# Kernel optimization log

Hardware: AMD Instinct MI355X
Metric: run time of the kernel (lower is better)

## Reference

```python
import jax, jax.numpy as jnp
import numpy as np
from jax import lax

N = 120000      # total real voxels
C = 128         # d_model
NH = 8          # heads
HD = C // NH    # head dim
T = 36          # window capacity
FILL = 24       # real tokens per window
NW = N // FILL  # 5000 windows
L = 4           # encoder layers (num_blocks=2, 2 layers each)
DFF = 256
B, H, Wd = 2, 320, 320
SCALE = HD ** -0.5


def setup_inputs() -> dict:
    key = jax.random.key(0)
    ks = jax.random.split(key, 16)
    voxel_feats = jax.random.normal(ks[0], (N, C), jnp.float32)
    # shift-0 window assignment: contiguous; shift-1: random permutation of voxels
    base = jnp.arange(N, dtype=jnp.int32)
    ind0 = (base // FILL) * T + (base % FILL)
    perm = jax.random.permutation(ks[1], N).astype(jnp.int32)
    ind1 = (perm // FILL) * T + (perm % FILL)
    mask = jnp.tile(jnp.arange(T) >= FILL, (NW, 1))  # True = padded key slot
    pos0 = 0.02 * jax.random.normal(ks[2], (NW, T, C), jnp.float32)
    pos1 = 0.02 * jax.random.normal(ks[3], (NW, T, C), jnp.float32)
    bcol = (jnp.arange(N) >= N // 2).astype(jnp.int32)
    yy = jax.random.randint(ks[4], (N,), 0, H, jnp.int32)
    xx = jax.random.randint(ks[5], (N,), 0, Wd, jnp.int32)
    voxel_coors = jnp.stack([bcol, jnp.zeros(N, jnp.int32), yy, xx], axis=1)
    s = 0.02
    return dict(
        voxel_feats=voxel_feats,
        pos0=pos0, pos1=pos1,
        in_proj_w=s * jax.random.normal(ks[6], (L, 3 * C, C), jnp.float32),
        in_proj_b=jnp.zeros((L, 3 * C), jnp.float32),
        out_proj_w=s * jax.random.normal(ks[7], (L, C, C), jnp.float32),
        out_proj_b=jnp.zeros((L, C), jnp.float32),
        lin1_w=s * jax.random.normal(ks[8], (L, DFF, C), jnp.float32),
        lin1_b=jnp.zeros((L, DFF), jnp.float32),
        lin2_w=s * jax.random.normal(ks[9], (L, C, DFF), jnp.float32),
        lin2_b=jnp.zeros((L, C), jnp.float32),
        ln1_w=jnp.ones((L, C), jnp.float32), ln1_b=jnp.zeros((L, C), jnp.float32),
        ln2_w=jnp.ones((L, C), jnp.float32), ln2_b=jnp.zeros((L, C), jnp.float32),
        conv_w=0.05 * jax.random.normal(ks[10], (2, C, C, 3, 3), jnp.float32),
        voxel_coors=voxel_coors, ind0=ind0, ind1=ind1, mask0=mask, mask1=mask,
    )


def _ln(x, w, b):
    m = jnp.mean(x, -1, keepdims=True)
    v = jnp.mean((x - m) ** 2, -1, keepdims=True)
    return (x - m) * lax.rsqrt(v + 1e-5) * w + b


def _encoder_layer(x, ind, pos, mask, ipw, ipb, opw, opb, l1w, l1b, l2w, l2b,
                   n1w, n1b, n2w, n2b):
    # flat2window_v2: scatter flat tokens into padded window buffer
    feat3d = jnp.zeros((NW * T, C), x.dtype).at[ind].set(x).reshape(NW, T, C)
    qk_in = feat3d + pos  # pos added to q and k only
    wq, wk, wv = ipw[:C], ipw[C:2 * C], ipw[2 * C:]
    bq, bk, bv = ipb[:C], ipb[C:2 * C], ipb[2 * C:]
    q = (qk_in @ wq.T + bq).reshape(NW, T, NH, HD)
    k = (qk_in @ wk.T + bk).reshape(NW, T, NH, HD)
    v = (feat3d @ wv.T + bv).reshape(NW, T, NH, HD)
    scores = jnp.einsum('wqhd,wkhd->whqk', q, k) * SCALE
    scores = jnp.where(mask[:, None, None, :], -1e9, scores)  # key padding mask
    attn = jax.nn.softmax(scores, axis=-1)
    o = jnp.einsum('whqk,wkhd->wqhd', attn, v).reshape(NW, T, C)
    o = o @ opw.T + opb
    a = o.reshape(NW * T, C)[ind]  # window2flat_v2: gather valid slots
    x = _ln(x + a, n1w, n1b)       # post_norm residual 1
    f = jax.nn.gelu(x @ l1w.T + l1b, approximate=False) @ l2w.T + l2b
    return _ln(x + f, n2w, n2b)    # post_norm residual 2


def reference(voxel_feats, pos0, pos1, in_proj_w, in_proj_b, out_proj_w,
              out_proj_b, lin1_w, lin1_b, lin2_w, lin2_b, ln1_w, ln1_b,
              ln2_w, ln2_b, conv_w, voxel_coors, ind0, ind1, mask0, mask1):
    x = voxel_feats
    for l in range(L):
        ind, pos, mask = (ind0, pos0, mask0) if l % 2 == 0 else (ind1, pos1, mask1)
        x = _encoder_layer(x, ind, pos, mask, in_proj_w[l], in_proj_b[l],
                           out_proj_w[l], out_proj_b[l], lin1_w[l], lin1_b[l],
                           lin2_w[l], lin2_b[l], ln1_w[l], ln1_b[l],
                           ln2_w[l], ln2_b[l])
    # recover_bev: scatter tokens into dense [B, C, H, W] canvas
    flat = voxel_coors[:, 2] * Wd + voxel_coors[:, 3]
    canvas = jnp.zeros((B, H * Wd, C), x.dtype).at[voxel_coors[:, 0], flat].set(x)
    out = canvas.reshape(B, H, Wd, C).transpose(0, 3, 1, 2)
    for i in range(2):  # attached 3x3 conv (bias=False) + ReLU
        out = jax.nn.relu(lax.conv_general_dilated(
            out, conv_w[i], (1, 1), [(1, 1), (1, 1)],
            dimension_numbers=('NCHW', 'OIHW', 'NCHW')))
    return out
```

## Files before the change

### kernel.cpp

```cpp
#include <hip/hip_runtime.h>
#include <math.h>

#define NVOX 120000
#define CDIM 128
#define NWIN 5000
#define HWPIX 102400

typedef __attribute__((ext_vector_type(8))) short short8;
typedef __attribute__((ext_vector_type(4))) float f32x4;

__device__ __forceinline__ unsigned short f2bf(float f) {
  unsigned u = __float_as_uint(f);
  return (unsigned short)((u + 0x7FFFu + ((u >> 16) & 1u)) >> 16);
}
__device__ __forceinline__ unsigned pack2(float a, float b) {
  return (unsigned)f2bf(a) | ((unsigned)f2bf(b) << 16);
}
__device__ __forceinline__ void unpack2(unsigned u, float& a, float& b) {
  a = __uint_as_float(u << 16);
  b = __uint_as_float(u & 0xFFFF0000u);
}

__device__ __forceinline__ void mma128(const short* __restrict__ As,
                                       const short* __restrict__ Ws,
                                       int aoff, int boff, f32x4 acc[2][4]) {
#pragma unroll
  for (int kc = 0; kc < 4; ++kc) {
    short8 a0 = *(const short8*)(As + aoff + kc * 32);
    short8 a1 = *(const short8*)(As + aoff + 136 * 16 + kc * 32);
#pragma unroll
    for (int nt = 0; nt < 4; ++nt) {
      short8 b = *(const short8*)(Ws + boff + nt * 136 * 16 + kc * 32);
      acc[0][nt] = __builtin_amdgcn_mfma_f32_16x16x32_bf16(a0, b, acc[0][nt], 0, 0, 0);
      acc[1][nt] = __builtin_amdgcn_mfma_f32_16x16x32_bf16(a1, b, acc[1][nt], 0, 0, 0);
    }
  }
}

__global__ __launch_bounds__(256) void cvt_kernel(const float* __restrict__ src,
                                                  unsigned short* __restrict__ dst, int n4) {
  int i = blockIdx.x * 256 + threadIdx.x;
  if (i >= n4) return;
  float4 v = ((const float4*)src)[i];
  uint2 o; o.x = pack2(v.x, v.y); o.y = pack2(v.z, v.w);
  ((uint2*)dst)[i] = o;
}

__global__ __launch_bounds__(256) void cvtT_kernel(const float* __restrict__ w,
                                                   unsigned short* __restrict__ wT) {
  int idx = blockIdx.x * 256 + threadIdx.x;
  if (idx >= 2 * 9 * 128 * 128) return;
  int ci = idx & 127;
  int co = (idx >> 7) & 127;
  int tap = (idx >> 14) % 9;
  int conv = idx / (9 * 16384);
  wT[idx] = f2bf(w[((size_t)(conv * 128 + co) * 128 + ci) * 9 + tap]);
}

__global__ __launch_bounds__(256) void qkv_kernel(
    const unsigned short* __restrict__ x, const float* __restrict__ pos,
    const int* __restrict__ ind, const unsigned short* __restrict__ ipwB,
    const float* __restrict__ ipb, unsigned short* __restrict__ qb,
    unsigned short* __restrict__ kb, unsigned short* __restrict__ vb) {
  __shared__ __align__(16) char ldsraw[52224];
  short* As = (short*)ldsraw;
  short* Ws = (short*)(ldsraw + 17408);
  const int t = threadIdx.x;
  const int lane = t & 63, wv = t >> 6;
  const int l15 = lane & 15, quad = lane >> 4;
  const int rbase = 32 * (wv >> 1), cbase = 64 * (wv & 1);
  const int mbase = blockIdx.x * 64;
  const int sec = blockIdx.y;
  f32x4 acc[2][4];
#pragma unroll
  for (int m = 0; m < 2; ++m)
#pragma unroll
    for (int n = 0; n < 4; ++n) acc[m][n] = (f32x4){0.f, 0.f, 0.f, 0.f};

  for (int fi = t; fi < 1024; fi += 256) {
    int row = fi >> 4, c8 = fi & 15;
    int vox = mbase + row;
    uint4 xv = ((const uint4*)x)[(size_t)vox * 16 + c8];
    if (sec < 2) {
      int s = ind[vox];
      const float4* pp = (const float4*)(pos + (size_t)s * 128 + c8 * 8);
      float4 p0 = pp[0], p1 = pp[1];
      float f0, f1, f2, f3, f4, f5, f6, f7;
      unpack2(xv.x, f0, f1); unpack2(xv.y, f2, f3);
      unpack2(xv.z, f4, f5); unpack2(xv.w, f6, f7);
      xv.x = pack2(f0 + p0.x, f1 + p0.y); xv.y = pack2(f2 + p0.z, f3 + p0.w);
      xv.z = pack2(f4 + p1.x, f5 + p1.y); xv.w = pack2(f6 + p1.z, f7 + p1.w);
    }
    *(uint4*)&As[row * 136 + c8 * 8] = xv;
  }
  for (int fi = t; fi < 2048; fi += 256) {
    int row = fi >> 4, c8 = fi & 15;
    ((uint4*)&Ws[row * 136])[c8] =
        ((const uint4*)(ipwB + (size_t)(sec * 128 + row) * 128))[c8];
  }
  __syncthreads();
  mma128(As, Ws, (rbase + l15) * 136 + quad * 8, (cbase + l15) * 136 + quad * 8, acc);
  __syncthreads();

  short* Ybf = (short*)ldsraw;
#pragma unroll
  for (int nt = 0; nt < 4; ++nt) {
    int col = cbase + nt * 16 + l15;
    float bias = ipb[sec * 128 + col];
#pragma unroll
    for (int mt = 0; mt < 2; ++mt)
#pragma unroll
      for (int r = 0; r < 4; ++r)
        Ybf[(rbase + mt * 16 + quad * 4 + r) * 136 + col] =
            (short)f2bf(acc[mt][nt][r] + bias);
  }
  __syncthreads();
  unsigned short* dst = (sec == 0) ? qb : ((sec == 1) ? kb : vb);
  for (int fi = t; fi < 1024; fi += 256) {
    int row = fi >> 4, c8 = fi & 15;
    int s = ind[mbase + row];
    int slot = (s / 36) * 24 + (s % 36);
    ((uint4*)dst)[(size_t)slot * 16 + c8] = ((const uint4*)&Ybf[row * 136])[c8];
  }
}

__global__ __launch_bounds__(256) void attn_kernel(
    unsigned short* __restrict__ qb, const unsigned short* __restrict__ kb,
    const unsigned short* __restrict__ vb) {
  __shared__ float lds[14112];
  float* Qs = lds;
  float* Ks = lds + 3168;
  float* Vs = lds + 6336;
  float* S = lds + 9504;
  const int t = threadIdx.x;
  const size_t base = (size_t)blockIdx.x * 3072;
  for (int fi = t; fi < 1152; fi += 256) {
    int arr = fi / 384, rem = fi % 384;
    int row = rem >> 4, c8 = rem & 15;
    const unsigned short* src = arr == 0 ? qb : (arr == 1 ? kb : vb);
    uint4 raw = ((const uint4*)(src + base))[row * 16 + c8];
    float* dl = lds + arr * 3168 + row * 132 + c8 * 8;
    unpack2(raw.x, dl[0], dl[1]); unpack2(raw.y, dl[2], dl[3]);
    unpack2(raw.z, dl[4], dl[5]); unpack2(raw.w, dl[6], dl[7]);
  }
  __syncthreads();
  for (int idx = t; idx < 4608; idx += 256) {
    int hh = idx / 576, rem = idx % 576;
    int qq = rem / 24, kk = rem % 24;
    const float* qp = &Qs[qq * 132 + hh * 16];
    const float* kp = &Ks[kk * 132 + hh * 16];
    float s = 0.f;
#pragma unroll
    for (int d = 0; d < 16; ++d) s = fmaf(qp[d], kp[d], s);
    S[idx] = s * 0.25f;
  }
  __syncthreads();
  if (t < 192) {
    float* rowp = &S[t * 24];
    float m = rowp[0];
#pragma unroll
    for (int k2 = 1; k2 < 24; ++k2) m = fmaxf(m, rowp[k2]);
    float sum = 0.f;
#pragma unroll
    for (int k2 = 0; k2 < 24; ++k2) { float e = __expf(rowp[k2] - m); rowp[k2] = e; sum += e; }
    float inv = 1.f / sum;
#pragma unroll
    for (int k2 = 0; k2 < 24; ++k2) rowp[k2] *= inv;
  }
  __syncthreads();
  for (int idx = t; idx < 3072; idx += 256) {
    int hh = idx / 384, rem = idx % 384;
    int qq = rem >> 4, dd = rem & 15;
    const float* pp = &S[hh * 576 + qq * 24];
    const float* vp = &Vs[hh * 16 + dd];
    float o = 0.f;
#pragma unroll
    for (int k2 = 0; k2 < 24; ++k2) o = fmaf(pp[k2], vp[k2 * 132], o);
    qb[base + qq * 128 + hh * 16 + dd] = f2bf(o);
  }
}

__global__ __launch_bounds__(256) void outln_kernel(
    const unsigned short* __restrict__ o, const int* __restrict__ ind,
    const unsigned short* __restrict__ opwB, const float* __restrict__ opb,
    const unsigned short* __restrict__ xres, const float* __restrict__ lnw,
    const float* __restrict__ lnb, unsigned short* __restrict__ hout) {
  __shared__ __align__(16) char ldsraw[52224];
  short* As = (short*)ldsraw;
  short* Ws = (short*)(ldsraw + 17408);
  const int t = threadIdx.x;
  const int lane = t & 63, wv = t >> 6;
  const int l15 = lane & 15, quad = lane >> 4;
  const int rbase = 32 * (wv >> 1), cbase = 64 * (wv & 1);
  const int mbase = blockIdx.x * 64;
  f32x4 acc[2][4];
#pragma unroll
  for (int m = 0; m < 2; ++m)
#pragma unroll
    for (int n = 0; n < 4; ++n) acc[m][n] = (f32x4){0.f, 0.f, 0.f, 0.f};

  for (int fi = t; fi < 1024; fi += 256) {
    int row = fi >> 4, c8 = fi & 15;
    int s = ind[mbase + row];
    int slot = (s / 36) * 24 + (s % 36);
    *(uint4*)&As[row * 136 + c8 * 8] = ((const uint4*)o)[(size_t)slot * 16 + c8];
  }
  for (int fi = t; fi < 2048; fi += 256) {
    int row = fi >> 4, c8 = fi & 15;
    ((uint4*)&Ws[row * 136])[c8] = ((const uint4*)(opwB + (size_t)row * 128))[c8];
  }
  __syncthreads();
  mma128(As, Ws, (rbase + l15) * 136 + quad * 8, (cbase + l15) * 136 + quad * 8, acc);
  __syncthreads();

  float* Yf = (float*)ldsraw;
  float* p1 = (float*)(ldsraw + 33792);
  float* p2 = (float*)(ldsraw + 34816);
  float* Ms = (float*)(ldsraw + 35840);
  float* Rs = (float*)(ldsraw + 36096);
#pragma unroll
  for (int nt = 0; nt < 4; ++nt) {
    int col = cbase + nt * 16 + l15;
    float bias = opb[col];
#pragma unroll
    for (int mt = 0; mt < 2; ++mt)
#pragma unroll
      for (int r = 0; r < 4; ++r)
        Yf[(rbase + mt * 16 + quad * 4 + r) * 132 + col] = acc[mt][nt][r] + bias;
  }
  __syncthreads();
  for (int fi = t; fi < 1024; fi += 256) {
    int row = fi >> 4, c8 = fi & 15;
    uint4 xv = ((const uint4*)xres)[(size_t)(mbase + row) * 16 + c8];
    float* yp = &Yf[row * 132 + c8 * 8];
    float a, b;
    unpack2(xv.x, a, b); yp[0] += a; yp[1] += b;
    unpack2(xv.y, a, b); yp[2] += a; yp[3] += b;
    unpack2(xv.z, a, b); yp[4] += a; yp[5] += b;
    unpack2(xv.w, a, b); yp[6] += a; yp[7] += b;
  }
  __syncthreads();
  {
    int r = t & 63, g = t >> 6;
    float s = 0.f, s2 = 0.f;
    for (int c = g * 32; c < g * 32 + 32; ++c) { float v = Yf[r * 132 + c]; s += v; s2 += v * v; }
    p1[g * 64 + r] = s; p2[g * 64 + r] = s2;
  }
  __syncthreads();
  if (t < 64) {
    float s = p1[t] + p1[64 + t] + p1[128 + t] + p1[192 + t];
    float s2 = p2[t] + p2[64 + t] + p2[128 + t] + p2[192 + t];
    float m = s * (1.f / 128.f);
    float var = s2 * (1.f / 128.f) - m * m;
    Ms[t] = m; Rs[t] = rsqrtf(var + 1e-5f);
  }
  __syncthreads();
  for (int fi = t; fi < 1024; fi += 256) {
    int row = fi >> 4, c8 = fi & 15;
    float m = Ms[row], rr = Rs[row];
    const float* yp = &Yf[row * 132 + c8 * 8];
    uint4 ov;
    float v0, v1;
#define LNPAIR(J, FLD) \
    v0 = (yp[2*J] - m) * rr * lnw[c8*8+2*J] + lnb[c8*8+2*J]; \
    v1 = (yp[2*J+1] - m) * rr * lnw[c8*8+2*J+1] + lnb[c8*8+2*J+1]; \
    ov.FLD = pack2(v0, v1);
    LNPAIR(0, x) LNPAIR(1, y) LNPAIR(2, z) LNPAIR(3, w)
#undef LNPAIR
    ((uint4*)hout)[(size_t)(mbase + row) * 16 + c8] = ov;
  }
}

__global__ __launch_bounds__(256) void ffn1_kernel(
    const unsigned short* __restrict__ h, const unsigned short* __restrict__ w1B,
    const float* __restrict__ b1, unsigned short* __restrict__ ff) {
  __shared__ __align__(16) char ldsraw[52224];
  short* As = (short*)ldsraw;
  short* Ws = (short*)(ldsraw + 17408);
  const int t = threadIdx.x;
  const int lane = t & 63, wv = t >> 6;
  const int l15 = lane & 15, quad = lane >> 4;
  const int rbase = 32 * (wv >> 1), cbase = 64 * (wv & 1);
  const int mbase = blockIdx.x * 64;
  const int by = blockIdx.y;
  f32x4 acc[2][4];
#pragma unroll
  for (int m = 0; m < 2; ++m)
#pragma unroll
    for (int n = 0; n < 4; ++n) acc[m][n] = (f32x4){0.f, 0.f, 0.f, 0.f};

  for (int fi = t; fi < 1024; fi += 256) {
    int row = fi >> 4, c8 = fi & 15;
    *(uint4*)&As[row * 136 + c8 * 8] = ((const uint4*)h)[(size_t)(mbase + row) * 16 + c8];
  }
  for (int fi = t; fi < 2048; fi += 256) {
    int row = fi >> 4, c8 = fi & 15;
    ((uint4*)&Ws[row * 136])[c8] =
        ((const uint4*)(w1B + (size_t)(by * 128 + row) * 128))[c8];
  }
  __syncthreads();
  mma128(As, Ws, (rbase + l15) * 136 + quad * 8, (cbase + l15) * 136 + quad * 8, acc);
  __syncthreads();

  short* Ybf = (short*)ldsraw;
#pragma unroll
  for (int nt = 0; nt < 4; ++nt) {
    int col = cbase + nt * 16 + l15;
    float bias = b1[by * 128 + col];
#pragma unroll
    for (int mt = 0; mt < 2; ++mt)
#pragma unroll
      for (int r = 0; r < 4; ++r) {
        float v = acc[mt][nt][r] + bias;
        float g = 0.5f * v * (1.f + erff(v * 0.70710678f));
        Ybf[(rbase + mt * 16 + quad * 4 + r) * 136 + col] = (short)f2bf(g);
      }
  }
  __syncthreads();
  for (int fi = t; fi < 1024; fi += 256) {
    int row = fi >> 4, c8 = fi & 15;
    ((uint4*)ff)[(size_t)(mbase + row) * 32 + by * 16 + c8] =
        ((const uint4*)&Ybf[row * 136])[c8];
  }
}

__global__ __launch_bounds__(256) void ffn2_kernel(
    const unsigned short* __restrict__ ff, const unsigned short* __restrict__ w2B,
    const float* __restrict__ b2, const unsigned short* __restrict__ hres,
    const float* __restrict__ lnw, const float* __restrict__ lnb,
    unsigned short* __restrict__ xout) {
  __shared__ __align__(16) char ldsraw[52224];
  short* As = (short*)ldsraw;
  short* Ws = (short*)(ldsraw + 17408);
  const int t = threadIdx.x;
  const int lane = t & 63, wv = t >> 6;
  const int l15 = lane & 15, quad = lane >> 4;
  const int rbase = 32 * (wv >> 1), cbase = 64 * (wv & 1);
  const int mbase = blockIdx.x * 64;
  f32x4 acc[2][4];
#pragma unroll
  for (int m = 0; m < 2; ++m)
#pragma unroll
    for (int n = 0; n < 4; ++n) acc[m][n] = (f32x4){0.f, 0.f, 0.f, 0.f};

  for (int k2 = 0; k2 < 2; ++k2) {
    if (k2) __syncthreads();
    for (int fi = t; fi < 1024; fi += 256) {
      int row = fi >> 4, c8 = fi & 15;
      *(uint4*)&As[row * 136 + c8 * 8] =
          ((const uint4*)ff)[(size_t)(mbase + row) * 32 + k2 * 16 + c8];
    }
    for (int fi = t; fi < 2048; fi += 256) {
      int row = fi >> 4, c8 = fi & 15;
      ((uint4*)&Ws[row * 136])[c8] =
          ((const uint4*)(w2B + (size_t)row * 256 + k2 * 128))[c8];
    }
    __syncthreads();
    mma128(As, Ws, (rbase + l15) * 136 + quad * 8, (cbase + l15) * 136 + quad * 8, acc);
  }
  __syncthreads();

  float* Yf = (float*)ldsraw;
  float* p1 = (float*)(ldsraw + 33792);
  float* p2 = (float*)(ldsraw + 34816);
  float* Ms = (float*)(ldsraw + 35840);
  float* Rs = (float*)(ldsraw + 36096);
#pragma unroll
  for (int nt = 0; nt < 4; ++nt) {
    int col = cbase + nt * 16 + l15;
    float bias = b2[col];
#pragma unroll
    for (int mt = 0; mt < 2; ++mt)
#pragma unroll
      for (int r = 0; r < 4; ++r)
        Yf[(rbase + mt * 16 + quad * 4 + r) * 132 + col] = acc[mt][nt][r] + bias;
  }
  __syncthreads();
  for (int fi = t; fi < 1024; fi += 256) {
    int row = fi >> 4, c8 = fi & 15;
    uint4 xv = ((const uint4*)hres)[(size_t)(mbase + row) * 16 + c8];
    float* yp = &Yf[row * 132 + c8 * 8];
    float a, b;
    unpack2(xv.x, a, b); yp[0] += a; yp[1] += b;
    unpack2(xv.y, a, b); yp[2] += a; yp[3] += b;
    unpack2(xv.z, a, b); yp[4] += a; yp[5] += b;
    unpack2(xv.w, a, b); yp[6] += a; yp[7] += b;
  }
  __syncthreads();
  {
    int r = t & 63, g = t >> 6;
    float s = 0.f, s2 = 0.f;
    for (int c = g * 32; c < g * 32 + 32; ++c) { float v = Yf[r * 132 + c]; s += v; s2 += v * v; }
    p1[g * 64 + r] = s; p2[g * 64 + r] = s2;
  }
  __syncthreads();
  if (t < 64) {
    float s = p1[t] + p1[64 + t] + p1[128 + t] + p1[192 + t];
    float s2 = p2[t] + p2[64 + t] + p2[128 + t] + p2[192 + t];
    float m = s * (1.f / 128.f);
    float var = s2 * (1.f / 128.f) - m * m;
    Ms[t] = m; Rs[t] = rsqrtf(var + 1e-5f);
  }
  __syncthreads();
  for (int fi = t; fi < 1024; fi += 256) {
    int row = fi >> 4, c8 = fi & 15;
    float m = Ms[row], rr = Rs[row];
    const float* yp = &Yf[row * 132 + c8 * 8];
    uint4 ov;
    float v0, v1;
#define LNPAIR(J, FLD) \
    v0 = (yp[2*J] - m) * rr * lnw[c8*8+2*J] + lnb[c8*8+2*J]; \
    v1 = (yp[2*J+1] - m) * rr * lnw[c8*8+2*J+1] + lnb[c8*8+2*J+1]; \
    ov.FLD = pack2(v0, v1);
    LNPAIR(0, x) LNPAIR(1, y) LNPAIR(2, z) LNPAIR(3, w)
#undef LNPAIR
    ((uint4*)xout)[(size_t)(mbase + row) * 16 + c8] = ov;
  }
}

__global__ void idx_init_kernel(int* __restrict__ idxmap) {
  int i = blockIdx.x * 256 + threadIdx.x;
  if (i < 2 * HWPIX) idxmap[i] = -1;
}

__global__ void scatter_kernel(const int* __restrict__ coors, int* __restrict__ idxmap) {
  int i = blockIdx.x * 256 + threadIdx.x;
  if (i >= NVOX) return;
  int b = coors[i * 4 + 0], y = coors[i * 4 + 2], xx = coors[i * 4 + 3];
  atomicMax(&idxmap[b * HWPIX + y * 320 + xx], i);
}

__global__ void canvas_kernel(const unsigned short* __restrict__ x,
                              const int* __restrict__ idxmap,
                              unsigned short* __restrict__ canvas) {
  int idx = blockIdx.x * 256 + threadIdx.x;
  if (idx >= 2 * HWPIX * 16) return;
  int cell = idx >> 4, c8 = idx & 15;
  int vox = idxmap[cell];
  uint4 v = {0u, 0u, 0u, 0u};
  if (vox >= 0) v = ((const uint4*)x)[(size_t)vox * 16 + c8];
  ((uint4*)canvas)[idx] = v;
}

template <int NCHW_OUT>
__global__ __launch_bounds__(256) void conv_kernel(
    const unsigned short* __restrict__ in, const unsigned short* __restrict__ wTb,
    void* __restrict__ outp) {
  __shared__ __align__(16) char ldsraw[52768];
  short* patch = (short*)ldsraw;
  short* Wt = (short*)(ldsraw + 17952);
  const int t = threadIdx.x;
  const int lane = t & 63, wv = t >> 6;
  const int l15 = lane & 15, quad = lane >> 4;
  const int rbase = 32 * (wv >> 1), cbase = 64 * (wv & 1);
  const int x0 = blockIdx.x * 64;
  const int y = blockIdx.y;
  const int b = blockIdx.z;
  const unsigned short* inb = in + (size_t)b * HWPIX * 128;
  f32x4 acc[2][4];
#pragma unroll
  for (int m = 0; m < 2; ++m)
#pragma unroll
    for (int n = 0; n < 4; ++n) acc[m][n] = (f32x4){0.f, 0.f, 0.f, 0.f};

  for (int dy = 0; dy < 3; ++dy) {
    __syncthreads();
    int gy = y + dy - 1;
    for (int fi = t; fi < 1056; fi += 256) {
      int col = fi >> 4, c8 = fi & 15;
      int gx = x0 + col - 1;
      uint4 v = {0u, 0u, 0u, 0u};
      if (gy >= 0 && gy < 320 && gx >= 0 && gx < 320)
        v = ((const uint4*)inb)[(size_t)(gy * 320 + gx) * 16 + c8];
      *(uint4*)&patch[col * 136 + c8 * 8] = v;
    }
    for (int dx = 0; dx < 3; ++dx) {
      __syncthreads();
      int tap = dy * 3 + dx;
      for (int fi = t; fi < 2048; fi += 256) {
        int row = fi >> 4, c8 = fi & 15;
        ((uint4*)&Wt[row * 136])[c8] =
            ((const uint4*)(wTb + (size_t)(tap * 128 + row) * 128))[c8];
      }
      __syncthreads();
      mma128(patch, Wt, (rbase + l15 + dx) * 136 + quad * 8,
             (cbase + l15) * 136 + quad * 8, acc);
    }
  }
  __syncthreads();
  if (NCHW_OUT) {
    float* Yf = (float*)ldsraw;
#pragma unroll
    for (int nt = 0; nt < 4; ++nt) {
      int col = cbase + nt * 16 + l15;
#pragma unroll
      for (int mt = 0; mt < 2; ++mt)
#pragma unroll
        for (int r = 0; r < 4; ++r)
          Yf[col * 68 + rbase + mt * 16 + quad * 4 + r] = fmaxf(acc[mt][nt][r], 0.f);
    }
    __syncthreads();
    float* out = (float*)outp;
    for (int fi = t; fi < 2048; fi += 256) {
      int co = fi >> 4, q4 = fi & 15;
      float4 v = *(float4*)&Yf[co * 68 + q4 * 4];
      *(float4*)&out[(size_t)(b * 128 + co) * HWPIX + y * 320 + x0 + q4 * 4] = v;
    }
  } else {
    short* Ybf = (short*)ldsraw;
#pragma unroll
    for (int nt = 0; nt < 4; ++nt) {
      int col = cbase + nt * 16 + l15;
#pragma unroll
      for (int mt = 0; mt < 2; ++mt)
#pragma unroll
        for (int r = 0; r < 4; ++r)
          Ybf[(rbase + mt * 16 + quad * 4 + r) * 136 + col] =
              (short)f2bf(fmaxf(acc[mt][nt][r], 0.f));
    }
    __syncthreads();
    unsigned short* out = (unsigned short*)outp;
    for (int fi = t; fi < 1024; fi += 256) {
      int row = fi >> 4, c8 = fi & 15;
      ((uint4*)out)[((size_t)b * HWPIX + y * 320 + x0 + row) * 16 + c8] =
          ((const uint4*)&Ybf[row * 136])[c8];
    }
  }
}

extern "C" void kernel_launch(void* const* d_in, const int* in_sizes, int n_in,
                              void* d_out, int out_size, void* d_ws, size_t ws_size,
                              hipStream_t stream) {
  const float* voxel_feats = (const float*)d_in[0];
  const float* pos0 = (const float*)d_in[1];
  const float* pos1 = (const float*)d_in[2];
  const float* ipw = (const float*)d_in[3];
  const float* ipb = (const float*)d_in[4];
  const float* opw = (const float*)d_in[5];
  const float* opb = (const float*)d_in[6];
  const float* l1w = (const float*)d_in[7];
  const float* l1b = (const float*)d_in[8];
  const float* l2w = (const float*)d_in[9];
  const float* l2b = (const float*)d_in[10];
  const float* n1w = (const float*)d_in[11];
  const float* n1b = (const float*)d_in[12];
  const float* n2w = (const float*)d_in[13];
  const float* n2b = (const float*)d_in[14];
  const float* convw = (const float*)d_in[15];
  const int* coors = (const int*)d_in[16];
  const int* ind0 = (const int*)d_in[17];
  const int* ind1 = (const int*)d_in[18];

  unsigned short* ws = (unsigned short*)d_ws;
  const size_t NC = (size_t)NVOX * CDIM;
  unsigned short* bx = ws;
  unsigned short* bq = ws + NC;
  unsigned short* bk = ws + 2 * NC;
  unsigned short* bv = ws + 3 * NC;
  unsigned short* bh = ws + 4 * NC;
  unsigned short* bff = ws + 5 * NC;
  unsigned short* wB = ws + 7 * NC;
  unsigned short* ipwB = wB;
  unsigned short* opwB = wB + 196608;
  unsigned short* l1wB = wB + 262144;
  unsigned short* l2wB = wB + 393216;
  unsigned short* convB = wB + 524288;
  int* idxmap = (int*)(wB + 819200);
  unsigned short* canvas = bq;
  unsigned short* c1out = bv;

  cvt_kernel<<<15000, 256, 0, stream>>>(voxel_feats, bx, 3840000);
  cvt_kernel<<<192, 256, 0, stream>>>(ipw, ipwB, 49152);
  cvt_kernel<<<64, 256, 0, stream>>>(opw, opwB, 16384);
  cvt_kernel<<<128, 256, 0, stream>>>(l1w, l1wB, 32768);
  cvt_kernel<<<128, 256, 0, stream>>>(l2w, l2wB, 32768);
  cvtT_kernel<<<1152, 256, 0, stream>>>(convw, convB);

  for (int l = 0; l < 4; ++l) {
    const int* ind = (l & 1) ? ind1 : ind0;
    const float* pos = (l & 1) ? pos1 : pos0;
    qkv_kernel<<<dim3(1875, 3), 256, 0, stream>>>(
        bx, pos, ind, ipwB + (size_t)l * 49152, ipb + l * 384, bq, bk, bv);
    attn_kernel<<<NWIN, 256, 0, stream>>>(bq, bk, bv);
    outln_kernel<<<1875, 256, 0, stream>>>(
        bq, ind, opwB + (size_t)l * 16384, opb + l * 128, bx,
        n1w + l * 128, n1b + l * 128, bh);
    ffn1_kernel<<<dim3(1875, 2), 256, 0, stream>>>(
        bh, l1wB + (size_t)l * 32768, l1b + l * 256, bff);
    ffn2_kernel<<<1875, 256, 0, stream>>>(
        bff, l2wB + (size_t)l * 32768, l2b + l * 128, bh,
        n2w + l * 128, n2b + l * 128, bx);
  }

  idx_init_kernel<<<800, 256, 0, stream>>>(idxmap);
  scatter_kernel<<<(NVOX + 255) / 256, 256, 0, stream>>>(coors, idxmap);
  canvas_kernel<<<12800, 256, 0, stream>>>(bx, idxmap, canvas);

  conv_kernel<0><<<dim3(5, 320, 2), 256, 0, stream>>>(canvas, convB, (void*)c1out);
  conv_kernel<1><<<dim3(5, 320, 2), 256, 0, stream>>>(c1out, convB + 9 * 16384, d_out);
}
```

Before: 1.610 ms.

## Loop QKV/FFN1 sections in-block, fuse attention per row, prefetch conv tiles

Several changes land together. The QKV and FFN1 kernels now loop over their output sections inside one block, so the activation tile is loaded once and the grid shrinks. Attention keeps scores in registers, with one thread per query/head doing QK, softmax and PV, which removes the LDS score buffer and two barriers. The conv kernel prefetches the next tap's weights and the next input row into registers while MFMA runs on the current ones. The cost is fewer blocks (less parallelism), only 192 active threads in attention, and higher register pressure in conv.

```diff
diff --git a/kernel.cpp b/kernel.cpp
--- a/kernel.cpp
+++ b/kernel.cpp
@@ -21,18 +21,23 @@
   b = __uint_as_float(u & 0xFFFF0000u);
 }
 
-__device__ __forceinline__ void mma128(const short* __restrict__ As,
-                                       const short* __restrict__ Ws,
-                                       int aoff, int boff, f32x4 acc[2][4]) {
+template <int MT>
+__device__ __forceinline__ void mma_k128(const short* __restrict__ As,
+                                         const short* __restrict__ Ws,
+                                         int aoff, int astride, int boff,
+                                         f32x4 acc[MT][4]) {
 #pragma unroll
   for (int kc = 0; kc < 4; ++kc) {
-    short8 a0 = *(const short8*)(As + aoff + kc * 32);
-    short8 a1 = *(const short8*)(As + aoff + 136 * 16 + kc * 32);
+    short8 a[MT];
+#pragma unroll
+    for (int mt = 0; mt < MT; ++mt)
+      a[mt] = *(const short8*)(As + aoff + mt * astride + kc * 32);
 #pragma unroll
     for (int nt = 0; nt < 4; ++nt) {
       short8 b = *(const short8*)(Ws + boff + nt * 136 * 16 + kc * 32);
-      acc[0][nt] = __builtin_amdgcn_mfma_f32_16x16x32_bf16(a0, b, acc[0][nt], 0, 0, 0);
-      acc[1][nt] = __builtin_amdgcn_mfma_f32_16x16x32_bf16(a1, b, acc[1][nt], 0, 0, 0);
+#pragma unroll
+      for (int mt = 0; mt < MT; ++mt)
+        acc[mt][nt] = __builtin_amdgcn_mfma_f32_16x16x32_bf16(a[mt], b, acc[mt][nt], 0, 0, 0);
     }
   }
 }
@@ -62,80 +67,90 @@
     const int* __restrict__ ind, const unsigned short* __restrict__ ipwB,
     const float* __restrict__ ipb, unsigned short* __restrict__ qb,
     unsigned short* __restrict__ kb, unsigned short* __restrict__ vb) {
-  __shared__ __align__(16) char ldsraw[52224];
+  __shared__ __align__(16) char ldsraw[52480];
   short* As = (short*)ldsraw;
   short* Ws = (short*)(ldsraw + 17408);
+  int* slots = (int*)(ldsraw + 52224);
   const int t = threadIdx.x;
   const int lane = t & 63, wv = t >> 6;
   const int l15 = lane & 15, quad = lane >> 4;
   const int rbase = 32 * (wv >> 1), cbase = 64 * (wv & 1);
   const int mbase = blockIdx.x * 64;
-  const int sec = blockIdx.y;
-  f32x4 acc[2][4];
-#pragma unroll
-  for (int m = 0; m < 2; ++m)
-#pragma unroll
-    for (int n = 0; n < 4; ++n) acc[m][n] = (f32x4){0.f, 0.f, 0.f, 0.f};
-
+
+  if (t < 64) {
+    int s = ind[mbase + t];
+    slots[t] = (s / 36) * 24 + (s % 36);
+  }
   for (int fi = t; fi < 1024; fi += 256) {
     int row = fi >> 4, c8 = fi & 15;
     int vox = mbase + row;
     uint4 xv = ((const uint4*)x)[(size_t)vox * 16 + c8];
-    if (sec < 2) {
-      int s = ind[vox];
-      const float4* pp = (const float4*)(pos + (size_t)s * 128 + c8 * 8);
-      float4 p0 = pp[0], p1 = pp[1];
-      float f0, f1, f2, f3, f4, f5, f6, f7;
-      unpack2(xv.x, f0, f1); unpack2(xv.y, f2, f3);
-      unpack2(xv.z, f4, f5); unpack2(xv.w, f6, f7);
-      xv.x = pack2(f0 + p0.x, f1 + p0.y); xv.y = pack2(f2 + p0.z, f3 + p0.w);
-      xv.z = pack2(f4 + p1.x, f5 + p1.y); xv.w = pack2(f6 + p1.z, f7 + p1.w);
-    }
+    int s = ind[vox];
+    const float4* pp = (const float4*)(pos + (size_t)s * 128 + c8 * 8);
+    float4 p0 = pp[0], p1 = pp[1];
+    float f0, f1, f2, f3, f4, f5, f6, f7;
+    unpack2(xv.x, f0, f1); unpack2(xv.y, f2, f3);
+    unpack2(xv.z, f4, f5); unpack2(xv.w, f6, f7);
+    xv.x = pack2(f0 + p0.x, f1 + p0.y); xv.y = pack2(f2 + p0.z, f3 + p0.w);
+    xv.z = pack2(f4 + p1.x, f5 + p1.y); xv.w = pack2(f6 + p1.z, f7 + p1.w);
     *(uint4*)&As[row * 136 + c8 * 8] = xv;
   }
-  for (int fi = t; fi < 2048; fi += 256) {
-    int row = fi >> 4, c8 = fi & 15;
-    ((uint4*)&Ws[row * 136])[c8] =
-        ((const uint4*)(ipwB + (size_t)(sec * 128 + row) * 128))[c8];
-  }
-  __syncthreads();
-  mma128(As, Ws, (rbase + l15) * 136 + quad * 8, (cbase + l15) * 136 + quad * 8, acc);
-  __syncthreads();
-
-  short* Ybf = (short*)ldsraw;
-#pragma unroll
-  for (int nt = 0; nt < 4; ++nt) {
-    int col = cbase + nt * 16 + l15;
-    float bias = ipb[sec * 128 + col];
-#pragma unroll
-    for (int mt = 0; mt < 2; ++mt)
-#pragma unroll
-      for (int r = 0; r < 4; ++r)
-        Ybf[(rbase + mt * 16 + quad * 4 + r) * 136 + col] =
-            (short)f2bf(acc[mt][nt][r] + bias);
-  }
-  __syncthreads();
-  unsigned short* dst = (sec == 0) ? qb : ((sec == 1) ? kb : vb);
-  for (int fi = t; fi < 1024; fi += 256) {
-    int row = fi >> 4, c8 = fi & 15;
-    int s = ind[mbase + row];
-    int slot = (s / 36) * 24 + (s % 36);
-    ((uint4*)dst)[(size_t)slot * 16 + c8] = ((const uint4*)&Ybf[row * 136])[c8];
+
+  for (int sec = 0; sec < 3; ++sec) {
+    if (sec == 2) {
+      for (int fi = t; fi < 1024; fi += 256) {
+        int row = fi >> 4, c8 = fi & 15;
+        *(uint4*)&As[row * 136 + c8 * 8] =
+            ((const uint4*)x)[(size_t)(mbase + row) * 16 + c8];
+      }
+    }
+    for (int fi = t; fi < 2048; fi += 256) {
+      int row = fi >> 4, c8 = fi & 15;
+      ((uint4*)&Ws[row * 136])[c8] =
+          ((const uint4*)(ipwB + (size_t)(sec * 128 + row) * 128))[c8];
+    }
+    __syncthreads();
+    f32x4 acc[2][4];
+#pragma unroll
+    for (int m = 0; m < 2; ++m)
+#pragma unroll
+      for (int n = 0; n < 4; ++n) acc[m][n] = (f32x4){0.f, 0.f, 0.f, 0.f};
+    mma_k128<2>(As, Ws, (rbase + l15) * 136 + quad * 8, 16 * 136,
+                (cbase + l15) * 136 + quad * 8, acc);
+    __syncthreads();
+    short* Ybf = Ws;
+#pragma unroll
+    for (int nt = 0; nt < 4; ++nt) {
+      int col = cbase + nt * 16 + l15;
+      float bias = ipb[sec * 128 + col];
+#pragma unroll
+      for (int mt = 0; mt < 2; ++mt)
+#pragma unroll
+        for (int r = 0; r < 4; ++r)
+          Ybf[(rbase + mt * 16 + quad * 4 + r) * 136 + col] =
+              (short)f2bf(acc[mt][nt][r] + bias);
+    }
+    __syncthreads();
+    unsigned short* dst = (sec == 0) ? qb : ((sec == 1) ? kb : vb);
+    for (int fi = t; fi < 1024; fi += 256) {
+      int row = fi >> 4, c8 = fi & 15;
+      ((uint4*)dst)[(size_t)slots[row] * 16 + c8] = ((const uint4*)&Ybf[row * 136])[c8];
+    }
+    __syncthreads();
   }
 }
 
 __global__ __launch_bounds__(256) void attn_kernel(
     unsigned short* __restrict__ qb, const unsigned short* __restrict__ kb,
     const unsigned short* __restrict__ vb) {
-  __shared__ float lds[14112];
+  __shared__ float lds[9504];
   float* Qs = lds;
   float* Ks = lds + 3168;
   float* Vs = lds + 6336;
-  float* S = lds + 9504;
   const int t = threadIdx.x;
   const size_t base = (size_t)blockIdx.x * 3072;
   for (int fi = t; fi < 1152; fi += 256) {
-    int arr = fi / 384, rem = fi % 384;
+    int arr = fi / 384, rem = fi - arr * 384;
     int row = rem >> 4, c8 = rem & 15;
     const unsigned short* src = arr == 0 ? qb : (arr == 1 ? kb : vb);
     uint4 raw = ((const uint4*)(src + base))[row * 16 + c8];
@@ -144,39 +159,55 @@
     unpack2(raw.z, dl[4], dl[5]); unpack2(raw.w, dl[6], dl[7]);
   }
   __syncthreads();
-  for (int idx = t; idx < 4608; idx += 256) {
-    int hh = idx / 576, rem = idx % 576;
-    int qq = rem / 24, kk = rem % 24;
-    const float* qp = &Qs[qq * 132 + hh * 16];
-    const float* kp = &Ks[kk * 132 + hh * 16];
-    float s = 0.f;
-#pragma unroll
-    for (int d = 0; d < 16; ++d) s = fmaf(qp[d], kp[d], s);
-    S[idx] = s * 0.25f;
-  }
-  __syncthreads();
   if (t < 192) {
-    float* rowp = &S[t * 24];
-    float m = rowp[0];
-#pragma unroll
-    for (int k2 = 1; k2 < 24; ++k2) m = fmaxf(m, rowp[k2]);
+    int h = t / 24, q = t - h * 24;
+    const float4* qp = (const float4*)&Qs[q * 132 + h * 16];
+    float4 q0 = qp[0], q1 = qp[1], q2 = qp[2], q3 = qp[3];
+    float sc[24];
+#pragma unroll
+    for (int k = 0; k < 24; ++k) {
+      const float4* kp = (const float4*)&Ks[k * 132 + h * 16];
+      float4 k0 = kp[0], k1 = kp[1], k2 = kp[2], k3 = kp[3];
+      float s = 0.f;
+      s = fmaf(q0.x, k0.x, s); s = fmaf(q0.y, k0.y, s);
+      s = fmaf(q0.z, k0.z, s); s = fmaf(q0.w, k0.w, s);
+      s = fmaf(q1.x, k1.x, s); s = fmaf(q1.y, k1.y, s);
+      s = fmaf(q1.z, k1.z, s); s = fmaf(q1.w, k1.w, s);
+      s = fmaf(q2.x, k2.x, s); s = fmaf(q2.y, k2.y, s);
+      s = fmaf(q2.z, k2.z, s); s = fmaf(q2.w, k2.w, s);
+      s = fmaf(q3.x, k3.x, s); s = fmaf(q3.y, k3.y, s);
+      s = fmaf(q3.z, k3.z, s); s = fmaf(q3.w, k3.w, s);
+      sc[k] = s * 0.25f;
+    }
+    float m = sc[0];
+#pragma unroll
+    for (int k = 1; k < 24; ++k) m = fmaxf(m, sc[k]);
     float sum = 0.f;
 #pragma unroll
-    for (int k2 = 0; k2 < 24; ++k2) { float e = __expf(rowp[k2] - m); rowp[k2] = e; sum += e; }
+    for (int k = 0; k < 24; ++k) { sc[k] = __expf(sc[k] - m); sum += sc[k]; }
     float inv = 1.f / sum;
-#pragma unroll
-    for (int k2 = 0; k2 < 24; ++k2) rowp[k2] *= inv;
-  }
-  __syncthreads();
-  for (int idx = t; idx < 3072; idx += 256) {
-    int hh = idx / 384, rem = idx % 384;
-    int qq = rem >> 4, dd = rem & 15;
-    const float* pp = &S[hh * 576 + qq * 24];
-    const float* vp = &Vs[hh * 16 + dd];
-    float o = 0.f;
-#pragma unroll
-    for (int k2 = 0; k2 < 24; ++k2) o = fmaf(pp[k2], vp[k2 * 132], o);
-    qb[base + qq * 128 + hh * 16 + dd] = f2bf(o);
+    float4 o0 = {0,0,0,0}, o1 = o0, o2 = o0, o3 = o0;
+#pragma unroll
+    for (int k = 0; k < 24; ++k) {
+      float p = sc[k] * inv;
+      const float4* vp = (const float4*)&Vs[k * 132 + h * 16];
+      float4 v0 = vp[0], v1 = vp[1], v2 = vp[2], v3 = vp[3];
+      o0.x = fmaf(p, v0.x, o0.x); o0.y = fmaf(p, v0.y, o0.y);
+      o0.z = fmaf(p, v0.z, o0.z); o0.w = fmaf(p, v0.w, o0.w);
+      o1.x = fmaf(p, v1.x, o1.x); o1.y = fmaf(p, v1.y, o1.y);
+      o1.z = fmaf(p, v1.z, o1.z); o1.w = fmaf(p, v1.w, o1.w);
+      o2.x = fmaf(p, v2.x, o2.x); o2.y = fmaf(p, v2.y, o2.y);
+      o2.z = fmaf(p, v2.z, o2.z); o2.w = fmaf(p, v2.w, o2.w);
+      o3.x = fmaf(p, v3.x, o3.x); o3.y = fmaf(p, v3.y, o3.y);
+      o3.z = fmaf(p, v3.z, o3.z); o3.w = fmaf(p, v3.w, o3.w);
+    }
+    uint4 lo, hi;
+    lo.x = pack2(o0.x, o0.y); lo.y = pack2(o0.z, o0.w);
+    lo.z = pack2(o1.x, o1.y); lo.w = pack2(o1.z, o1.w);
+    hi.x = pack2(o2.x, o2.y); hi.y = pack2(o2.z, o2.w);
+    hi.z = pack2(o3.x, o3.y); hi.w = pack2(o3.z, o3.w);
+    ((uint4*)(qb + base))[q * 16 + h * 2] = lo;
+    ((uint4*)(qb + base))[q * 16 + h * 2 + 1] = hi;
   }
 }
 
@@ -210,7 +241,8 @@
     ((uint4*)&Ws[row * 136])[c8] = ((const uint4*)(opwB + (size_t)row * 128))[c8];
   }
   __syncthreads();
-  mma128(As, Ws, (rbase + l15) * 136 + quad * 8, (cbase + l15) * 136 + quad * 8, acc);
+  mma_k128<2>(As, Ws, (rbase + l15) * 136 + quad * 8, 16 * 136,
+              (cbase + l15) * 136 + quad * 8, acc);
   __syncthreads();
 
   float* Yf = (float*)ldsraw;
@@ -282,45 +314,47 @@
   const int l15 = lane & 15, quad = lane >> 4;
   const int rbase = 32 * (wv >> 1), cbase = 64 * (wv & 1);
   const int mbase = blockIdx.x * 64;
-  const int by = blockIdx.y;
-  f32x4 acc[2][4];
-#pragma unroll
-  for (int m = 0; m < 2; ++m)
-#pragma unroll
-    for (int n = 0; n < 4; ++n) acc[m][n] = (f32x4){0.f, 0.f, 0.f, 0.f};
 
   for (int fi = t; fi < 1024; fi += 256) {
     int row = fi >> 4, c8 = fi & 15;
     *(uint4*)&As[row * 136 + c8 * 8] = ((const uint4*)h)[(size_t)(mbase + row) * 16 + c8];
   }
-  for (int fi = t; fi < 2048; fi += 256) {
-    int row = fi >> 4, c8 = fi & 15;
-    ((uint4*)&Ws[row * 136])[c8] =
-        ((const uint4*)(w1B + (size_t)(by * 128 + row) * 128))[c8];
-  }
-  __syncthreads();
-  mma128(As, Ws, (rbase + l15) * 136 + quad * 8, (cbase + l15) * 136 + quad * 8, acc);
-  __syncthreads();
-
-  short* Ybf = (short*)ldsraw;
-#pragma unroll
-  for (int nt = 0; nt < 4; ++nt) {
-    int col = cbase + nt * 16 + l15;
-    float bias = b1[by * 128 + col];
-#pragma unroll
-    for (int mt = 0; mt < 2; ++mt)
-#pragma unroll
-      for (int r = 0; r < 4; ++r) {
-        float v = acc[mt][nt][r] + bias;
-        float g = 0.5f * v * (1.f + erff(v * 0.70710678f));
-        Ybf[(rbase + mt * 16 + quad * 4 + r) * 136 + col] = (short)f2bf(g);
-      }
-  }
-  __syncthreads();
-  for (int fi = t; fi < 1024; fi += 256) {
-    int row = fi >> 4, c8 = fi & 15;
-    ((uint4*)ff)[(size_t)(mbase + row) * 32 + by * 16 + c8] =
-        ((const uint4*)&Ybf[row * 136])[c8];
+  for (int by = 0; by < 2; ++by) {
+    for (int fi = t; fi < 2048; fi += 256) {
+      int row = fi >> 4, c8 = fi & 15;
+      ((uint4*)&Ws[row * 136])[c8] =
+          ((const uint4*)(w1B + (size_t)(by * 128 + row) * 128))[c8];
+    }
+    __syncthreads();
+    f32x4 acc[2][4];
+#pragma unroll
+    for (int m = 0; m < 2; ++m)
+#pragma unroll
+      for (int n = 0; n < 4; ++n) acc[m][n] = (f32x4){0.f, 0.f, 0.f, 0.f};
+    mma_k128<2>(As, Ws, (rbase + l15) * 136 + quad * 8, 16 * 136,
+                (cbase + l15) * 136 + quad * 8, acc);
+    __syncthreads();
+    short* Ybf = Ws;
+#pragma unroll
+    for (int nt = 0; nt < 4; ++nt) {
+      int col = cbase + nt * 16 + l15;
+      float bias = b1[by * 128 + col];
+#pragma unroll
+      for (int mt = 0; mt < 2; ++mt)
+#pragma unroll
+        for (int r = 0; r < 4; ++r) {
+          float v = acc[mt][nt][r] + bias;
+          float g = 0.5f * v * (1.f + erff(v * 0.70710678f));
+          Ybf[(rbase + mt * 16 + quad * 4 + r) * 136 + col] = (short)f2bf(g);
+        }
+    }
+    __syncthreads();
+    for (int fi = t; fi < 1024; fi += 256) {
+      int row = fi >> 4, c8 = fi & 15;
+      ((uint4*)ff)[(size_t)(mbase + row) * 32 + by * 16 + c8] =
+          ((const uint4*)&Ybf[row * 136])[c8];
+    }
+    __syncthreads();
   }
 }
 
@@ -356,7 +390,8 @@
           ((const uint4*)(w2B + (size_t)row * 256 + k2 * 128))[c8];
     }
     __syncthreads();
-    mma128(As, Ws, (rbase + l15) * 136 + quad * 8, (cbase + l15) * 136 + quad * 8, acc);
+    mma_k128<2>(As, Ws, (rbase + l15) * 136 + quad * 8, 16 * 136,
+                (cbase + l15) * 136 + quad * 8, acc);
   }
   __syncthreads();
 
@@ -448,7 +483,7 @@
     void* __restrict__ outp) {
   __shared__ __align__(16) char ldsraw[52768];
   short* patch = (short*)ldsraw;
-  short* Wt = (short*)(ldsraw + 17952);
+  short* Ws = (short*)(ldsraw + 17952);
   const int t = threadIdx.x;
   const int lane = t & 63, wv = t >> 6;
   const int l15 = lane & 15, quad = lane >> 4;
@@ -463,31 +498,80 @@
 #pragma unroll
     for (int n = 0; n < 4; ++n) acc[m][n] = (f32x4){0.f, 0.f, 0.f, 0.f};
 
+  uint4 wreg[8], preg[5];
+#pragma unroll
+  for (int u = 0; u < 8; ++u) {
+    int fi = t + 256 * u;
+    wreg[u] = ((const uint4*)(wTb + (size_t)(fi >> 4) * 128))[fi & 15];
+  }
+  {
+    int gy = y - 1;
+#pragma unroll
+    for (int u = 0; u < 5; ++u) {
+      int fi = t + 256 * u;
+      preg[u] = (uint4){0u, 0u, 0u, 0u};
+      if (fi < 1056) {
+        int gx = x0 + (fi >> 4) - 1;
+        if (gy >= 0 && gy < 320 && gx >= 0 && gx < 320)
+          preg[u] = ((const uint4*)inb)[(size_t)(gy * 320 + gx) * 16 + (fi & 15)];
+      }
+    }
+  }
+#pragma unroll
+  for (int u = 0; u < 8; ++u) {
+    int fi = t + 256 * u;
+    *(uint4*)&Ws[(fi >> 4) * 136 + (fi & 15) * 8] = wreg[u];
+  }
+#pragma unroll
+  for (int u = 0; u < 5; ++u) {
+    int fi = t + 256 * u;
+    if (fi < 1056) *(uint4*)&patch[(fi >> 4) * 136 + (fi & 15) * 8] = preg[u];
+  }
+  __syncthreads();
+
   for (int dy = 0; dy < 3; ++dy) {
-    __syncthreads();
-    int gy = y + dy - 1;
-    for (int fi = t; fi < 1056; fi += 256) {
-      int col = fi >> 4, c8 = fi & 15;
-      int gx = x0 + col - 1;
-      uint4 v = {0u, 0u, 0u, 0u};
-      if (gy >= 0 && gy < 320 && gx >= 0 && gx < 320)
-        v = ((const uint4*)inb)[(size_t)(gy * 320 + gx) * 16 + c8];
-      *(uint4*)&patch[col * 136 + c8 * 8] = v;
+    if (dy < 2) {
+      int gy = y + dy;
+#pragma unroll
+      for (int u = 0; u < 5; ++u) {
+        int fi = t + 256 * u;
+        preg[u] = (uint4){0u, 0u, 0u, 0u};
+        if (fi < 1056) {
+          int gx = x0 + (fi >> 4) - 1;
+          if (gy >= 0 && gy < 320 && gx >= 0 && gx < 320)
+            preg[u] = ((const uint4*)inb)[(size_t)(gy * 320 + gx) * 16 + (fi & 15)];
+        }
+      }
     }
     for (int dx = 0; dx < 3; ++dx) {
+      int tap = dy * 3 + dx;
+      if (tap < 8) {
+#pragma unroll
+        for (int u = 0; u < 8; ++u) {
+          int fi = t + 256 * u;
+          wreg[u] = ((const uint4*)(wTb + (size_t)((tap + 1) * 128 + (fi >> 4)) * 128))[fi & 15];
+        }
+      }
+      mma_k128<2>(patch, Ws, (rbase + l15 + dx) * 136 + quad * 8, 16 * 136,
+                  (cbase + l15) * 136 + quad * 8, acc);
       __syncthreads();
-      int tap = dy * 3 + dx;
-      for (int fi = t; fi < 2048; fi += 256) {
-        int row = fi >> 4, c8 = fi & 15;
-        ((uint4*)&Wt[row * 136])[c8] =
-            ((const uint4*)(wTb + (size_t)(tap * 128 + row) * 128))[c8];
+      if (tap < 8) {
+#pragma unroll
+        for (int u = 0; u < 8; ++u) {
+          int fi = t + 256 * u;
+          *(uint4*)&Ws[(fi >> 4) * 136 + (fi & 15) * 8] = wreg[u];
+        }
+      }
+      if (dx == 2 && dy < 2) {
+#pragma unroll
+        for (int u = 0; u < 5; ++u) {
+          int fi = t + 256 * u;
+          if (fi < 1056) *(uint4*)&patch[(fi >> 4) * 136 + (fi & 15) * 8] = preg[u];
+        }
       }
       __syncthreads();
-      mma128(patch, Wt, (rbase + l15 + dx) * 136 + quad * 8,
-             (cbase + l15) * 136 + quad * 8, acc);
-    }
-  }
-  __syncthreads();
+    }
+  }
   if (NCHW_OUT) {
     float* Yf = (float*)ldsraw;
 #pragma unroll
@@ -579,13 +663,13 @@
   for (int l = 0; l < 4; ++l) {
     const int* ind = (l & 1) ? ind1 : ind0;
     const float* pos = (l & 1) ? pos1 : pos0;
-    qkv_kernel<<<dim3(1875, 3), 256, 0, stream>>>(
+    qkv_kernel<<<1875, 256, 0, stream>>>(
         bx, pos, ind, ipwB + (size_t)l * 49152, ipb + l * 384, bq, bk, bv);
     attn_kernel<<<NWIN, 256, 0, stream>>>(bq, bk, bv);
     outln_kernel<<<1875, 256, 0, stream>>>(
         bq, ind, opwB + (size_t)l * 16384, opb + l * 128, bx,
         n1w + l * 128, n1b + l * 128, bh);
-    ffn1_kernel<<<dim3(1875, 2), 256, 0, stream>>>(
+    ffn1_kernel<<<1875, 256, 0, stream>>>(
         bh, l1wB + (size_t)l * 32768, l1b + l * 256, bff);
     ffn2_kernel<<<1875, 256, 0, stream>>>(
         bff, l2wB + (size_t)l * 32768, l2b + l * 128, bh,
```

Measured after the change: 1.629 ms. No clear change (+1.2%).
